# Kernel tuning notes

Hardware: AMD Instinct MI355X
Metric: run time of the kernel (lower is better)

## Reference

```python
import jax, jax.numpy as jnp
import numpy as np

B, S, DIM = 2, 2048, 1536
H = 12            # n_heads (SIGMA)
HD = DIM // H     # head_dim = 128
SIGMA = 12        # anchors per query: 6 local + 4 strided + 2 global
STRIDE_STEP = 5   # SOPFR


def setup_inputs() -> dict:
    key = jax.random.key(0)
    k0, k1, k2 = jax.random.split(key, 3)
    s = 0.02
    return {
        "x": jax.random.normal(k0, (B, S, DIM), dtype=jnp.float32),
        "Wqkv": jax.random.normal(k1, (DIM, 3 * DIM), dtype=jnp.float32) * s,
        "bqkv": jnp.zeros((3 * DIM,), dtype=jnp.float32),
        "Wout": jax.random.normal(k2, (DIM, DIM), dtype=jnp.float32) * s,
        "bout": jnp.zeros((DIM,), dtype=jnp.float32),
        # Egyptian-fraction init: [W_LOCAL, W_STRIDE, W_GLOBAL] = [1/2, 1/3, 1/6]
        "group_scale": jnp.array([0.5, 1.0 / 3.0, 1.0 / 6.0], dtype=jnp.float32),
    }


def _anchor_indices(seq_len):
    # (S, 12) int32: 6 local offsets, 4 strided offsets, then global {0, S-1}
    pos = jnp.arange(seq_len, dtype=jnp.int32)
    offs = jnp.array([-3, -2, -1, 1, 2, 3,
                      -2 * STRIDE_STEP, -STRIDE_STEP, STRIDE_STEP, 2 * STRIDE_STEP],
                     dtype=jnp.int32)
    a = jnp.clip(pos[:, None] + offs[None, :], 0, seq_len - 1)
    glob = jnp.stack([jnp.zeros_like(pos), jnp.full_like(pos, seq_len - 1)], axis=1)
    return jnp.concatenate([a, glob], axis=1)


def reference(x, Wqkv, bqkv, Wout, bout, group_scale):
    b, s, d_model = x.shape
    # QKV projection -> (3, B, H, S, HD)
    qkv = (x @ Wqkv + bqkv).reshape(b, s, 3, H, HD).transpose(2, 0, 3, 1, 4)
    q, k, v = qkv[0], qkv[1], qkv[2]
    scale = HD ** -0.5

    anchor = _anchor_indices(s)                 # (S, SIGMA)
    k_anchors = jnp.take(k, anchor, axis=2)     # (B, H, S, SIGMA, HD)
    v_anchors = jnp.take(v, anchor, axis=2)     # (B, H, S, SIGMA, HD)

    attn = jnp.einsum('bhsd,bhsad->bhsa', q, k_anchors) * scale

    gw = jax.nn.softmax(group_scale)            # (3,)
    weight_per_anchor = jnp.concatenate([
        jnp.broadcast_to(gw[0], (6,)),   # local
        jnp.broadcast_to(gw[1], (4,)),   # strided
        jnp.broadcast_to(gw[2], (2,)),   # global
    ])                                          # (SIGMA,)
    attn = attn + jnp.log(weight_per_anchor)    # broadcast over (B,H,S,·)

    attn = jax.nn.softmax(attn, axis=-1)
    attn = jnp.nan_to_num(attn, nan=0.0)

    out = jnp.einsum('bhsa,bhsad->bhsd', attn, v_anchors)
    out = out.transpose(0, 2, 1, 3).reshape(b, s, d_model)
    return out @ Wout + bout
```

## Files before the change

### kernel.cpp

```cpp
#include <hip/hip_runtime.h>
#include <hip/hip_bf16.h>
#include <cstdint>
#include <math.h>

#define B_    2
#define S_    2048
#define DIM_  1536
#define H_    12
#define HD_   128
#define TRI_  4608
#define M_    4096

typedef __attribute__((ext_vector_type(8)))  __bf16 bf16x8;
typedef __attribute__((ext_vector_type(4)))  __bf16 bf16x4;
typedef __attribute__((ext_vector_type(4)))  float  floatx4;
typedef __attribute__((ext_vector_type(16))) float  floatx16;

typedef __attribute__((address_space(3))) uint8_t       lds_u8;
typedef const __attribute__((address_space(1))) uint8_t glob_u8;

__global__ __launch_bounds__(256) void prep(const float* __restrict__ W1,
                                            __bf16* __restrict__ O1,
                                            const float* __restrict__ W2,
                                            __bf16* __restrict__ O2,
                                            const float* __restrict__ x,
                                            __bf16* __restrict__ x_bf) {
    const int T1 = (TRI_ / 64) * (DIM_ / 64);
    const int T2 = (DIM_ / 64) * (DIM_ / 64);
    int blk = blockIdx.x;
    const int t = threadIdx.x;

    if (blk >= T1 + T2) {
        blk -= T1 + T2;
        int i = blk * 256 + t;
        float4 v = ((const float4*)x)[i];
        bf16x4 o;
        o.x = (__bf16)v.x; o.y = (__bf16)v.y; o.z = (__bf16)v.z; o.w = (__bf16)v.w;
        *(bf16x4*)(x_bf + (size_t)i * 4) = o;
        return;
    }

    const float* in; __bf16* out; int R, C, c0, r0;
    if (blk < T1) {
        in = W1; out = O1; R = DIM_; C = TRI_;
        c0 = (blk % (TRI_ / 64)) * 64; r0 = (blk / (TRI_ / 64)) * 64;
    } else {
        blk -= T1;
        in = W2; out = O2; R = DIM_; C = DIM_;
        c0 = (blk % (DIM_ / 64)) * 64; r0 = (blk / (DIM_ / 64)) * 64;
    }
    __shared__ float tile[64][65];
    const int c4 = t & 15, r = t >> 4;
    #pragma unroll
    for (int i = 0; i < 64; i += 16) {
        float4 v = *(const float4*)&in[(size_t)(r0 + r + i) * C + c0 + c4 * 4];
        tile[r + i][c4 * 4 + 0] = v.x;
        tile[r + i][c4 * 4 + 1] = v.y;
        tile[r + i][c4 * 4 + 2] = v.z;
        tile[r + i][c4 * 4 + 3] = v.w;
    }
    __syncthreads();
    const int cc = t >> 2, ch = t & 3;
    #pragma unroll
    for (int cho = 0; cho < 8; cho += 4) {
        int chh = ch + cho;
        bf16x8 o;
        #pragma unroll
        for (int k = 0; k < 8; ++k) o[k] = (__bf16)tile[chh * 8 + k][cc];
        *(bf16x8*)&out[(size_t)(c0 + cc) * R + r0 + chh * 8] = o;
    }
}

__global__ __launch_bounds__(256, 3) void gemm_qkv(const __bf16* __restrict__ A,
                                                   const __bf16* __restrict__ Bt,
                                                   const float*  __restrict__ bias,
                                                   __bf16* __restrict__ Cout,
                                                   int Mdim, int Ndim, int Kdim) {
    __shared__ __align__(16) __bf16 sA[128 * 64];
    __shared__ __align__(16) __bf16 sB[192 * 64];

    const int ntiles = Ndim / 192;
    const int tile_n = blockIdx.x % ntiles;
    const int tile_m = blockIdx.x / ntiles;
    const int m0 = tile_m << 7, n0 = tile_n * 192;

    const int tid  = threadIdx.x;
    const int lane = tid & 63;
    const int wave = tid >> 6;
    const int wm = (wave >> 1) * 64;
    const int wn = (wave & 1) * 96;

    floatx16 acc[2][3] = {};

    const int lr8 = lane >> 3;
    const int swz = (((lane & 7) ^ lr8) * 8);

    const int m32  = lane & 31;
    const int half = lane >> 5;
    const int lx7  = lane & 7;

    for (int k0 = 0; k0 < Kdim; k0 += 64) {
        #pragma unroll
        for (int c = 0; c < 4; ++c) {
            int r0 = wave * 32 + c * 8;
            const __bf16* ga = A + (size_t)(m0 + r0 + lr8) * Kdim + k0 + swz;
            __builtin_amdgcn_global_load_lds((glob_u8*)ga, (lds_u8*)&sA[r0 * 64], 16, 0, 0);
        }
        #pragma unroll
        for (int c = 0; c < 6; ++c) {
            int r0 = wave * 48 + c * 8;
            const __bf16* gb = Bt + (size_t)(n0 + r0 + lr8) * Kdim + k0 + swz;
            __builtin_amdgcn_global_load_lds((glob_u8*)gb, (lds_u8*)&sB[r0 * 64], 16, 0, 0);
        }
        __syncthreads();

        #pragma unroll
        for (int ks = 0; ks < 4; ++ks) {
            const int ko = (((ks * 2 + half) ^ lx7) * 8);
            bf16x8 af[2], bfr[3];
            #pragma unroll
            for (int i = 0; i < 2; ++i)
                af[i] = *(const bf16x8*)&sA[(wm + i * 32 + m32) * 64 + ko];
            #pragma unroll
            for (int j = 0; j < 3; ++j)
                bfr[j] = *(const bf16x8*)&sB[(wn + j * 32 + m32) * 64 + ko];
            #pragma unroll
            for (int i = 0; i < 2; ++i)
                #pragma unroll
                for (int j = 0; j < 3; ++j)
                    acc[i][j] = __builtin_amdgcn_mfma_f32_32x32x16_bf16(af[i], bfr[j], acc[i][j], 0, 0, 0);
        }
        __syncthreads();
    }

    #pragma unroll
    for (int j = 0; j < 3; ++j) {
        int gc = n0 + wn + j * 32 + m32;
        float bv = bias[gc];
        #pragma unroll
        for (int i = 0; i < 2; ++i) {
            #pragma unroll
            for (int r = 0; r < 16; ++r) {
                int gr = m0 + wm + i * 32 + (r & 3) + 8 * (r >> 2) + 4 * half;
                Cout[(size_t)gr * Ndim + gc] = (__bf16)(acc[i][j][r] + bv);
            }
        }
    }
}

__global__ __launch_bounds__(256, 3) void gemm_out(const __bf16* __restrict__ A,
                                                   const __bf16* __restrict__ Bt,
                                                   const float*  __restrict__ bias,
                                                   float* __restrict__ Cout,
                                                   int Mdim, int Ndim, int Kdim) {
    __shared__ __align__(16) __bf16 sA[64 * 128];
    __shared__ __align__(16) __bf16 sB[128 * 128];

    const int ntiles = Ndim >> 7;
    const int tile_n = blockIdx.x % ntiles;
    const int tile_m = blockIdx.x / ntiles;
    const int m0 = tile_m << 6, n0 = tile_n << 7;

    const int tid  = threadIdx.x;
    const int lane = tid & 63;
    const int wave = tid >> 6;
    const int wm = (wave >> 1) * 32;
    const int wn = (wave & 1) * 64;

    floatx4 acc[2][4] = {};

    const int lr4 = lane >> 4;
    const int lc  = lane & 15;
    int swz[4];
    #pragma unroll
    for (int v = 0; v < 4; ++v) swz[v] = (lc ^ (v * 4 + lr4)) * 8;

    const int row  = lane & 15;
    const int quad = lane >> 4;

    for (int k0 = 0; k0 < Kdim; k0 += 128) {
        #pragma unroll
        for (int c = 0; c < 4; ++c) {
            int r0 = wave * 16 + c * 4;
            const __bf16* ga = A + (size_t)(m0 + r0 + lr4) * Kdim + k0 + swz[c & 3];
            __builtin_amdgcn_global_load_lds((glob_u8*)ga, (lds_u8*)&sA[r0 * 128], 16, 0, 0);
        }
        #pragma unroll
        for (int c = 0; c < 8; ++c) {
            int r0 = wave * 32 + c * 4;
            const __bf16* gb = Bt + (size_t)(n0 + r0 + lr4) * Kdim + k0 + swz[c & 3];
            __builtin_amdgcn_global_load_lds((glob_u8*)gb, (lds_u8*)&sB[r0 * 128], 16, 0, 0);
        }
        __syncthreads();

        #pragma unroll
        for (int ks = 0; ks < 4; ++ks) {
            const int ck = ((ks * 4 + quad) ^ row) * 8;
            bf16x8 af[2], bfr[4];
            #pragma unroll
            for (int i = 0; i < 2; ++i)
                af[i]  = *(const bf16x8*)&sA[(wm + i * 16 + row) * 128 + ck];
            #pragma unroll
            for (int j = 0; j < 4; ++j)
                bfr[j] = *(const bf16x8*)&sB[(wn + j * 16 + row) * 128 + ck];
            #pragma unroll
            for (int i = 0; i < 2; ++i)
                #pragma unroll
                for (int j = 0; j < 4; ++j)
                    acc[i][j] = __builtin_amdgcn_mfma_f32_16x16x32_bf16(af[i], bfr[j], acc[i][j], 0, 0, 0);
        }
        __syncthreads();
    }

    #pragma unroll
    for (int j = 0; j < 4; ++j) {
        int gc = n0 + wn + j * 16 + row;
        float bv = bias[gc];
        #pragma unroll
        for (int i = 0; i < 2; ++i) {
            #pragma unroll
            for (int r = 0; r < 4; ++r) {
                int gr = m0 + wm + i * 16 + quad * 4 + r;
                Cout[(size_t)gr * Ndim + gc] = acc[i][j][r] + bv;
            }
        }
    }
}

#define AROWS 86
#define ATOT  2752

__global__ __launch_bounds__(256) void anchor_attn(const __bf16* __restrict__ qkv,
                                                   const float* __restrict__ group_scale,
                                                   __bf16* __restrict__ attn_out) {
    const int sc = blockIdx.x;
    const int h  = blockIdx.y;
    const int b  = blockIdx.z;
    const int s0 = sc * 64;

    __shared__ __align__(16) __bf16 sKV[2 * AROWS * 128];

    const int tid  = threadIdx.x;
    const int wave = tid >> 6;

    #pragma unroll
    for (int base = 0; base < ATOT; base += 256) {
        int i = base + tid;
        if (i < ATOT) {
            int r  = i >> 4;
            int c  = i & 15;
            int kv = (r >= AROWS) ? 1 : 0;
            int rr = r - AROWS * kv;
            int s_row = (rr < 84) ? min(max(s0 - 10 + rr, 0), S_ - 1)
                                  : (rr == 84 ? 0 : S_ - 1);
            int cs = c ^ (rr & 7);
            const __bf16* src = qkv + (size_t)(b * S_ + s_row) * TRI_
                              + DIM_ * (1 + kv) + h * HD_ + cs * 8;
            __builtin_amdgcn_global_load_lds((glob_u8*)src,
                (lds_u8*)sKV + (size_t)(base + wave * 64) * 16, 16, 0, 0);
        }
    }

    float g0 = group_scale[0], g1 = group_scale[1], g2 = group_scale[2];
    float gm = fmaxf(g0, fmaxf(g1, g2));
    float e0 = __expf(g0 - gm), e1 = __expf(g1 - gm), e2 = __expf(g2 - gm);
    float ls = __logf(e0 + e1 + e2);
    float lw0 = g0 - gm - ls, lw1 = g1 - gm - ls, lw2 = g2 - gm - ls;

    const int s_local = tid >> 2;
    const int ds      = tid & 3;
    const int s       = s0 + s_local;

    float q[32];
    {
        const __bf16* qp = qkv + (size_t)(b * S_ + s) * TRI_ + h * HD_ + ds * 32;
        #pragma unroll
        for (int j = 0; j < 4; ++j) {
            bf16x8 qv = *(const bf16x8*)(qp + j * 8);
            #pragma unroll
            for (int k = 0; k < 8; ++k) q[j * 8 + k] = (float)qv[k];
        }
    }

    int slot[12];
    const int offs[10] = {-3, -2, -1, 1, 2, 3, -10, -5, 5, 10};
    #pragma unroll
    for (int a = 0; a < 10; ++a) slot[a] = s_local + 10 + offs[a];
    slot[10] = 84; slot[11] = 85;

    __syncthreads();

    const float scale = 0.08838834764831845f;
    float p[12];
    float mx = -1e30f;
    #pragma unroll
    for (int a = 0; a < 12; ++a) {
        const int ro = slot[a] * 128;
        const int sw = slot[a] & 7;
        float d = 0.f;
        #pragma unroll
        for (int j = 0; j < 4; ++j) {
            bf16x8 kv = *(const bf16x8*)&sKV[ro + ((ds * 4 + j) ^ sw) * 8];
            #pragma unroll
            for (int k = 0; k < 8; ++k) d += q[j * 8 + k] * (float)kv[k];
        }
        d += __shfl_xor(d, 1); d += __shfl_xor(d, 2);
        float v = d * scale + (a < 6 ? lw0 : (a < 10 ? lw1 : lw2));
        p[a] = v;
        mx = fmaxf(mx, v);
    }
    float l = 0.f;
    #pragma unroll
    for (int a = 0; a < 12; ++a) { p[a] = __expf(p[a] - mx); l += p[a]; }
    float inv = 1.0f / l;

    float o[32] = {};
    #pragma unroll
    for (int a = 0; a < 12; ++a) {
        const int ro = AROWS * 128 + slot[a] * 128;
        const int sw = slot[a] & 7;
        float pa = p[a];
        #pragma unroll
        for (int j = 0; j < 4; ++j) {
            bf16x8 vv = *(const bf16x8*)&sKV[ro + ((ds * 4 + j) ^ sw) * 8];
            #pragma unroll
            for (int k = 0; k < 8; ++k) o[j * 8 + k] += pa * (float)vv[k];
        }
    }

    __bf16* op = attn_out + (size_t)(b * S_ + s) * DIM_ + h * HD_ + ds * 32;
    #pragma unroll
    for (int j = 0; j < 4; ++j) {
        bf16x8 ov;
        #pragma unroll
        for (int k = 0; k < 8; ++k) ov[k] = (__bf16)(o[j * 8 + k] * inv);
        *(bf16x8*)(op + j * 8) = ov;
    }
}

extern "C" void kernel_launch(void* const* d_in, const int* in_sizes, int n_in,
                              void* d_out, int out_size, void* d_ws, size_t ws_size,
                              hipStream_t stream) {
    const float* x    = (const float*)d_in[0];
    const float* Wqkv = (const float*)d_in[1];
    const float* bqkv = (const float*)d_in[2];
    const float* Wout = (const float*)d_in[3];
    const float* bout = (const float*)d_in[4];
    const float* gsc  = (const float*)d_in[5];
    float* out = (float*)d_out;

    char* ws = (char*)d_ws;
    __bf16* x_bf   = (__bf16*)(ws);
    __bf16* WqkvT  = (__bf16*)(ws + 12582912);
    __bf16* WoutT  = (__bf16*)(ws + 12582912 + 14155776);
    __bf16* qkv    = (__bf16*)(ws + 12582912 + 14155776 + 4718592);
    __bf16* attn   = (__bf16*)(ws + 12582912 + 14155776 + 4718592 + 37748736);

    {
        int nblk = (TRI_ / 64) * (DIM_ / 64) + (DIM_ / 64) * (DIM_ / 64)
                 + (M_ * DIM_) / 1024;
        prep<<<nblk, 256, 0, stream>>>(Wqkv, WqkvT, Wout, WoutT, x, x_bf);
    }

    gemm_qkv<<<(M_ / 128) * (TRI_ / 192), 256, 0, stream>>>(
        x_bf, WqkvT, bqkv, qkv, M_, TRI_, DIM_);

    anchor_attn<<<dim3(32, H_, B_), 256, 0, stream>>>(qkv, gsc, attn);

    gemm_out<<<(M_ / 64) * (DIM_ / 128), 256, 0, stream>>>(
        attn, WoutT, bout, out, M_, DIM_, DIM_);
}
```

Before: 210.1 us.

## Double-buffer LDS staging in QKV and output GEMMs

Both GEMM kernels now use two LDS buffers and prefetch the next K-slice with global_load_lds while MFMAs consume the current one. This drops one barrier per iteration and overlaps global loads with compute. The output GEMM's K tile shrinks from 128 to 64, with a matching 8-wide swizzle, to keep its LDS footprint the same. The QKV GEMM doubles its LDS use and lowers launch_bounds occupancy from 3 to 2 blocks per CU, so it trades latency hiding across blocks for latency hiding within a block.

After: 226.0 us. 1.08x slower.

```diff
diff --git a/kernel.cpp b/kernel.cpp
--- a/kernel.cpp
+++ b/kernel.cpp
@@ -71,13 +71,13 @@
     }
 }
 
-__global__ __launch_bounds__(256, 3) void gemm_qkv(const __bf16* __restrict__ A,
+__global__ __launch_bounds__(256, 2) void gemm_qkv(const __bf16* __restrict__ A,
                                                    const __bf16* __restrict__ Bt,
                                                    const float*  __restrict__ bias,
                                                    __bf16* __restrict__ Cout,
                                                    int Mdim, int Ndim, int Kdim) {
-    __shared__ __align__(16) __bf16 sA[128 * 64];
-    __shared__ __align__(16) __bf16 sB[192 * 64];
+    __shared__ __align__(16) __bf16 sA[2][128 * 64];
+    __shared__ __align__(16) __bf16 sB[2][192 * 64];
 
     const int ntiles = Ndim / 192;
     const int tile_n = blockIdx.x % ntiles;
@@ -99,20 +99,26 @@
     const int half = lane >> 5;
     const int lx7  = lane & 7;
 
-    for (int k0 = 0; k0 < Kdim; k0 += 64) {
+    auto stage = [&](int buf, int kk) {
         #pragma unroll
         for (int c = 0; c < 4; ++c) {
             int r0 = wave * 32 + c * 8;
-            const __bf16* ga = A + (size_t)(m0 + r0 + lr8) * Kdim + k0 + swz;
-            __builtin_amdgcn_global_load_lds((glob_u8*)ga, (lds_u8*)&sA[r0 * 64], 16, 0, 0);
+            const __bf16* ga = A + (size_t)(m0 + r0 + lr8) * Kdim + kk + swz;
+            __builtin_amdgcn_global_load_lds((glob_u8*)ga, (lds_u8*)&sA[buf][r0 * 64], 16, 0, 0);
         }
         #pragma unroll
         for (int c = 0; c < 6; ++c) {
             int r0 = wave * 48 + c * 8;
-            const __bf16* gb = Bt + (size_t)(n0 + r0 + lr8) * Kdim + k0 + swz;
-            __builtin_amdgcn_global_load_lds((glob_u8*)gb, (lds_u8*)&sB[r0 * 64], 16, 0, 0);
-        }
+            const __bf16* gb = Bt + (size_t)(n0 + r0 + lr8) * Kdim + kk + swz;
+            __builtin_amdgcn_global_load_lds((glob_u8*)gb, (lds_u8*)&sB[buf][r0 * 64], 16, 0, 0);
+        }
+    };
+
+    stage(0, 0);
+    for (int k0 = 0; k0 < Kdim; k0 += 64) {
+        const int cur = (k0 >> 6) & 1;
         __syncthreads();
+        if (k0 + 64 < Kdim) stage(cur ^ 1, k0 + 64);
 
         #pragma unroll
         for (int ks = 0; ks < 4; ++ks) {
@@ -120,17 +126,16 @@
             bf16x8 af[2], bfr[3];
             #pragma unroll
             for (int i = 0; i < 2; ++i)
-                af[i] = *(const bf16x8*)&sA[(wm + i * 32 + m32) * 64 + ko];
+                af[i] = *(const bf16x8*)&sA[cur][(wm + i * 32 + m32) * 64 + ko];
             #pragma unroll
             for (int j = 0; j < 3; ++j)
-                bfr[j] = *(const bf16x8*)&sB[(wn + j * 32 + m32) * 64 + ko];
+                bfr[j] = *(const bf16x8*)&sB[cur][(wn + j * 32 + m32) * 64 + ko];
             #pragma unroll
             for (int i = 0; i < 2; ++i)
                 #pragma unroll
                 for (int j = 0; j < 3; ++j)
                     acc[i][j] = __builtin_amdgcn_mfma_f32_32x32x16_bf16(af[i], bfr[j], acc[i][j], 0, 0, 0);
         }
-        __syncthreads();
     }
 
     #pragma unroll
@@ -153,8 +158,8 @@
                                                    const float*  __restrict__ bias,
                                                    float* __restrict__ Cout,
                                                    int Mdim, int Ndim, int Kdim) {
-    __shared__ __align__(16) __bf16 sA[64 * 128];
-    __shared__ __align__(16) __bf16 sB[128 * 128];
+    __shared__ __align__(16) __bf16 sA[2][64 * 64];
+    __shared__ __align__(16) __bf16 sB[2][128 * 64];
 
     const int ntiles = Ndim >> 7;
     const int tile_n = blockIdx.x % ntiles;
@@ -169,47 +174,49 @@
 
     floatx4 acc[2][4] = {};
 
-    const int lr4 = lane >> 4;
-    const int lc  = lane & 15;
-    int swz[4];
-    #pragma unroll
-    for (int v = 0; v < 4; ++v) swz[v] = (lc ^ (v * 4 + lr4)) * 8;
+    const int lr8 = lane >> 3;
+    const int swz = ((lane & 7) ^ lr8) * 8;
 
     const int row  = lane & 15;
     const int quad = lane >> 4;
 
-    for (int k0 = 0; k0 < Kdim; k0 += 128) {
+    auto stage = [&](int buf, int kk) {
+        #pragma unroll
+        for (int c = 0; c < 2; ++c) {
+            int r0 = wave * 16 + c * 8;
+            const __bf16* ga = A + (size_t)(m0 + r0 + lr8) * Kdim + kk + swz;
+            __builtin_amdgcn_global_load_lds((glob_u8*)ga, (lds_u8*)&sA[buf][r0 * 64], 16, 0, 0);
+        }
         #pragma unroll
         for (int c = 0; c < 4; ++c) {
-            int r0 = wave * 16 + c * 4;
-            const __bf16* ga = A + (size_t)(m0 + r0 + lr4) * Kdim + k0 + swz[c & 3];
-            __builtin_amdgcn_global_load_lds((glob_u8*)ga, (lds_u8*)&sA[r0 * 128], 16, 0, 0);
-        }
-        #pragma unroll
-        for (int c = 0; c < 8; ++c) {
-            int r0 = wave * 32 + c * 4;
-            const __bf16* gb = Bt + (size_t)(n0 + r0 + lr4) * Kdim + k0 + swz[c & 3];
-            __builtin_amdgcn_global_load_lds((glob_u8*)gb, (lds_u8*)&sB[r0 * 128], 16, 0, 0);
-        }
+            int r0 = wave * 32 + c * 8;
+            const __bf16* gb = Bt + (size_t)(n0 + r0 + lr8) * Kdim + kk + swz;
+            __builtin_amdgcn_global_load_lds((glob_u8*)gb, (lds_u8*)&sB[buf][r0 * 64], 16, 0, 0);
+        }
+    };
+
+    stage(0, 0);
+    for (int k0 = 0; k0 < Kdim; k0 += 64) {
+        const int cur = (k0 >> 6) & 1;
         __syncthreads();
-
-        #pragma unroll
-        for (int ks = 0; ks < 4; ++ks) {
-            const int ck = ((ks * 4 + quad) ^ row) * 8;
+        if (k0 + 64 < Kdim) stage(cur ^ 1, k0 + 64);
+
+        #pragma unroll
+        for (int ks = 0; ks < 2; ++ks) {
+            const int ck = ((ks * 4 + quad) ^ (row & 7)) * 8;
             bf16x8 af[2], bfr[4];
             #pragma unroll
             for (int i = 0; i < 2; ++i)
-                af[i]  = *(const bf16x8*)&sA[(wm + i * 16 + row) * 128 + ck];
+                af[i]  = *(const bf16x8*)&sA[cur][(wm + i * 16 + row) * 64 + ck];
             #pragma unroll
             for (int j = 0; j < 4; ++j)
-                bfr[j] = *(const bf16x8*)&sB[(wn + j * 16 + row) * 128 + ck];
+                bfr[j] = *(const bf16x8*)&sB[cur][(wn + j * 16 + row) * 64 + ck];
             #pragma unroll
             for (int i = 0; i < 2; ++i)
                 #pragma unroll
                 for (int j = 0; j < 4; ++j)
                     acc[i][j] = __builtin_amdgcn_mfma_f32_16x16x32_bf16(af[i], bfr[j], acc[i][j], 0, 0, 0);
         }
-        __syncthreads();
     }
 
     #pragma unroll
```
